# Performance work log

Measured on AMD Instinct MI355X. Metric: run time of the kernel, lower is better.

## Reference

```python
import jax, jax.numpy as jnp
import numpy as np

B, T, F, H = 2048, 256, 128, 64


def setup_inputs() -> dict:
    key = jax.random.key(0)
    ks = jax.random.split(key, 7)
    s_ih = 1.0 / np.sqrt(H)
    return {
        "x": jax.random.normal(ks[0], (B, T, F), dtype=jnp.float32),
        "w_ih": jax.random.uniform(ks[1], (3 * H, F), jnp.float32, -s_ih, s_ih),
        "w_hh": jax.random.uniform(ks[2], (3 * H, H), jnp.float32, -s_ih, s_ih),
        "b_ih": jax.random.uniform(ks[3], (3 * H,), jnp.float32, -s_ih, s_ih),
        "b_hh": jax.random.uniform(ks[4], (3 * H,), jnp.float32, -s_ih, s_ih),
        "fc_w": jax.random.uniform(ks[5], (1, H), jnp.float32, -s_ih, s_ih),
        "fc_b": jax.random.uniform(ks[6], (1,), jnp.float32, -s_ih, s_ih),
    }


def _gru_last_hidden(x, w_ih, w_hh, b_ih, b_hh):
    # Precompute input projections for all timesteps: [B,T,3H] -> scan over T
    gx = jnp.einsum("btf,gf->btg", x, w_ih) + b_ih  # g = 3H
    gx = jnp.transpose(gx, (1, 0, 2))  # [T, B, 3H]
    h0 = jnp.zeros((x.shape[0], w_hh.shape[1]), dtype=x.dtype)
    Hd = w_hh.shape[1]

    def step(h, gx_t):
        gh = h @ w_hh.T + b_hh  # [B, 3H]
        rx, zx, nx = gx_t[:, :Hd], gx_t[:, Hd:2 * Hd], gx_t[:, 2 * Hd:]
        rh, zh, nh = gh[:, :Hd], gh[:, Hd:2 * Hd], gh[:, 2 * Hd:]
        r = jax.nn.sigmoid(rx + rh)
        z = jax.nn.sigmoid(zx + zh)
        n = jnp.tanh(nx + r * nh)
        h_new = (1.0 - z) * n + z * h
        return h_new, None

    h_last, _ = jax.lax.scan(step, h0, gx)
    return h_last  # [B, H]


def reference(x, w_ih, w_hh, b_ih, b_hh, fc_w, fc_b):
    # eval mode: dropout is identity
    h_last = _gru_last_hidden(x, w_ih, w_hh, b_ih, b_hh)
    return h_last @ fc_w.T + fc_b  # [B, 1]
```

## Files before the change

kernel.cpp:

```cpp
#include <hip/hip_runtime.h>

#define B_ 2048
#define T_ 256
#define F_ 128
#define H_ 64

typedef __attribute__((ext_vector_type(8))) short short8;
typedef __attribute__((ext_vector_type(4))) float f32x4;

__device__ __forceinline__ unsigned int rne2(float fa, float fb) {
    unsigned int ua = __float_as_uint(fa);
    unsigned int ub = __float_as_uint(fb);
    ua = ua + 0x7fffu + ((ua >> 16) & 1u);
    ub = ub + 0x7fffu + ((ub >> 16) & 1u);
    return (ua >> 16) | (ub & 0xffff0000u);
}
__device__ __forceinline__ float sigmoid_f(float v) {
    return __fdividef(1.0f, 1.0f + __expf(-v));
}
__device__ __forceinline__ float tanh_f(float v) {
    return 1.0f - __fdividef(2.0f, 1.0f + __expf(2.0f * v));
}

__global__ __launch_bounds__(128, 2) void gru_fused(
    const float* __restrict__ x, const float* __restrict__ w_ih,
    const float* __restrict__ w_hh, const float* __restrict__ b_ih,
    const float* __restrict__ b_hh, const float* __restrict__ fc_w,
    const float* __restrict__ fc_b, float* __restrict__ out)
{
    __shared__ __align__(16) short wihf[12 * 4 * 64 * 8];
    __shared__ __align__(16) short whhf[12 * 2 * 64 * 8];
    __shared__ __align__(16) short hhi_l[2][4][72];
    __shared__ __align__(16) short hlo_l[2][4][72];
    __shared__ float wred[2][4];

    const int tid = threadIdx.x;
    const int wv  = tid >> 6;
    const int j   = tid & 63;
    const int q   = j >> 4;
    const int c   = j & 15;
    const int brow = blockIdx.x * 4;

    for (int s = tid; s < 12 * 4 * 64; s += 128) {
        const int n = s >> 8, ks = (s >> 6) & 3, L = s & 63;
        const float* wp = w_ih + (n * 16 + (L & 15)) * F_ + ks * 32 + ((L >> 4) * 8);
        const float4 a = *(const float4*)wp;
        const float4 b = *(const float4*)(wp + 4);
        union { short8 v; unsigned int u[4]; } fr;
        fr.u[0] = rne2(a.x, a.y); fr.u[1] = rne2(a.z, a.w);
        fr.u[2] = rne2(b.x, b.y); fr.u[3] = rne2(b.z, b.w);
        *(short8*)&wihf[s * 8] = fr.v;
    }
    for (int s = tid; s < 12 * 2 * 64; s += 128) {
        const int n = s >> 7, ks2 = (s >> 6) & 1, L = s & 63;
        const float* wp = w_hh + (n * 16 + (L & 15)) * H_ + ks2 * 32 + ((L >> 4) * 8);
        const float4 a = *(const float4*)wp;
        const float4 b = *(const float4*)(wp + 4);
        union { short8 v; unsigned int u[4]; } fr;
        fr.u[0] = rne2(a.x, a.y); fr.u[1] = rne2(a.z, a.w);
        fr.u[2] = rne2(b.x, b.y); fr.u[3] = rne2(b.z, b.w);
        *(short8*)&whhf[s * 8] = fr.v;
    }
    for (int i = tid; i < 2 * 4 * 72; i += 128) {
        ((short*)hhi_l)[i] = 0;
        ((short*)hlo_l)[i] = 0;
    }

    const int d0 = wv * 32 + c;
    float bxr[2], bxz[2], bxn[2], bgr[2], bgz[2], bgn[2];
    #pragma unroll
    for (int n2 = 0; n2 < 2; ++n2) {
        const int d = d0 + n2 * 16;
        bxr[n2] = b_ih[d];        bgr[n2] = b_hh[d];
        bxz[n2] = b_ih[64 + d];   bgz[n2] = b_hh[64 + d];
        bxn[n2] = b_ih[128 + d];  bgn[n2] = b_hh[128 + d];
    }
    const float fw0 = fc_w[d0], fw1 = fc_w[d0 + 16];

    const int xrow = (j & 15) & 3;
    const int xsl  = (j & 15) >> 3;
    const float* xlane = x + ((size_t)(brow + xrow) * T_ + xsl) * F_ + q * 8;

    __syncthreads();

    float4 XA[8], XB[8];
    {
        const float* lp = xlane;
        #pragma unroll
        for (int ks = 0; ks < 4; ++ks) {
            XA[2 * ks]     = *(const float4*)(lp + ks * 32);
            XA[2 * ks + 1] = *(const float4*)(lp + ks * 32 + 4);
        }
        lp = xlane + 2 * F_;
        #pragma unroll
        for (int ks = 0; ks < 4; ++ks) {
            XB[2 * ks]     = *(const float4*)(lp + ks * 32);
            XB[2 * ks + 1] = *(const float4*)(lp + ks * 32 + 4);
        }
    }

    short8 af[4], hh[2], hl[2];
    const short8 z8 = {0, 0, 0, 0, 0, 0, 0, 0};
    hh[0] = z8; hh[1] = z8; hl[0] = z8; hl[1] = z8;

    auto cvtbuf = [&](float4 (&Xv)[8]) {
        #pragma unroll
        for (int ks = 0; ks < 4; ++ks) {
            union { short8 v; unsigned int u[4]; } fr;
            fr.u[0] = rne2(Xv[2 * ks].x,     Xv[2 * ks].y);
            fr.u[1] = rne2(Xv[2 * ks].z,     Xv[2 * ks].w);
            fr.u[2] = rne2(Xv[2 * ks + 1].x, Xv[2 * ks + 1].y);
            fr.u[3] = rne2(Xv[2 * ks + 1].z, Xv[2 * ks + 1].w);
            af[ks] = fr.v;
        }
    };
    cvtbuf(XA);

    auto do_macro = [&](float4 (&Xre)[8], float4 (&Xcv)[8], int t0) {
        f32x4 axr[2], axz[2], axn[2];
        #pragma unroll
        for (int n2 = 0; n2 < 2; ++n2) {
            axr[n2] = (f32x4){bxr[n2], bxr[n2], bxr[n2], bxr[n2]};
            axz[n2] = (f32x4){bxz[n2], bxz[n2], bxz[n2], bxz[n2]};
            axn[n2] = (f32x4){bxn[n2], bxn[n2], bxn[n2], bxn[n2]};
            const int tr = (0 + wv * 2 + n2) * 2048;
            const int tz = (4 + wv * 2 + n2) * 2048;
            const int tn = (8 + wv * 2 + n2) * 2048;
            #pragma unroll
            for (int ks = 0; ks < 4; ++ks) {
                axr[n2] = __builtin_amdgcn_mfma_f32_16x16x32_bf16(
                    af[ks], *(const short8*)&wihf[tr + ks * 512 + j * 8], axr[n2], 0, 0, 0);
                axz[n2] = __builtin_amdgcn_mfma_f32_16x16x32_bf16(
                    af[ks], *(const short8*)&wihf[tz + ks * 512 + j * 8], axz[n2], 0, 0, 0);
                axn[n2] = __builtin_amdgcn_mfma_f32_16x16x32_bf16(
                    af[ks], *(const short8*)&wihf[tn + ks * 512 + j * 8], axn[n2], 0, 0, 0);
            }
        }
        {
            int tl = t0 + 4; if (tl > 254) tl = 254;
            const float* lp = xlane + (size_t)tl * F_;
            #pragma unroll
            for (int ks = 0; ks < 4; ++ks) {
                Xre[2 * ks]     = *(const float4*)(lp + ks * 32);
                Xre[2 * ks + 1] = *(const float4*)(lp + ks * 32 + 4);
            }
        }
        auto step = [&](int s) {
            f32x4 agr[2], agz[2], agn[2];
            #pragma unroll
            for (int n2 = 0; n2 < 2; ++n2) {
                agr[n2] = (f32x4){bgr[n2], bgr[n2], bgr[n2], bgr[n2]};
                agz[n2] = (f32x4){bgz[n2], bgz[n2], bgz[n2], bgz[n2]};
                agn[n2] = (f32x4){bgn[n2], bgn[n2], bgn[n2], bgn[n2]};
                const int tr = (0 + wv * 2 + n2) * 1024;
                const int tz = (4 + wv * 2 + n2) * 1024;
                const int tn = (8 + wv * 2 + n2) * 1024;
                #pragma unroll
                for (int ks2 = 0; ks2 < 2; ++ks2) {
                    const short8 br = *(const short8*)&whhf[tr + ks2 * 512 + j * 8];
                    const short8 bz = *(const short8*)&whhf[tz + ks2 * 512 + j * 8];
                    const short8 bn = *(const short8*)&whhf[tn + ks2 * 512 + j * 8];
                    agr[n2] = __builtin_amdgcn_mfma_f32_16x16x32_bf16(hh[ks2], br, agr[n2], 0, 0, 0);
                    agr[n2] = __builtin_amdgcn_mfma_f32_16x16x32_bf16(hl[ks2], br, agr[n2], 0, 0, 0);
                    agz[n2] = __builtin_amdgcn_mfma_f32_16x16x32_bf16(hh[ks2], bz, agz[n2], 0, 0, 0);
                    agz[n2] = __builtin_amdgcn_mfma_f32_16x16x32_bf16(hl[ks2], bz, agz[n2], 0, 0, 0);
                    agn[n2] = __builtin_amdgcn_mfma_f32_16x16x32_bf16(hh[ks2], bn, agn[n2], 0, 0, 0);
                    agn[n2] = __builtin_amdgcn_mfma_f32_16x16x32_bf16(hl[ks2], bn, agn[n2], 0, 0, 0);
                }
            }
            if ((q >> 1) == s) {
                const int rowsel = q & 1;
                #pragma unroll
                for (int n2 = 0; n2 < 2; ++n2) {
                    const int d = d0 + n2 * 16;
                    #pragma unroll
                    for (int rl = 0; rl < 2; ++rl) {
                        const int row = rowsel * 2 + rl;
                        const float vr  = rowsel ? axr[n2][2 + rl] + agr[n2][2 + rl]
                                                 : axr[n2][rl]     + agr[n2][rl];
                        const float vz  = rowsel ? axz[n2][2 + rl] + agz[n2][2 + rl]
                                                 : axz[n2][rl]     + agz[n2][rl];
                        const float vnx = rowsel ? axn[n2][2 + rl] : axn[n2][rl];
                        const float vnh = rowsel ? agn[n2][2 + rl] : agn[n2][rl];
                        const float r = sigmoid_f(vr);
                        const float z = sigmoid_f(vz);
                        const float n = tanh_f(vnx + r * vnh);
                        const float hp =
                            __uint_as_float(((unsigned int)(unsigned short)hhi_l[s][row][d]) << 16) +
                            __uint_as_float(((unsigned int)(unsigned short)hlo_l[s][row][d]) << 16);
                        const float hn = n + z * (hp - n);
                        const unsigned int uh = __float_as_uint(hn);
                        const unsigned int rr = uh + 0x7fffu + ((uh >> 16) & 1u);
                        const float hif = __uint_as_float(rr & 0xffff0000u);
                        const float lof = hn - hif;
                        const unsigned int ul = __float_as_uint(lof);
                        const unsigned int r2 = ul + 0x7fffu + ((ul >> 16) & 1u);
                        hhi_l[s ^ 1][row][d] = (short)(rr >> 16);
                        hlo_l[s ^ 1][row][d] = (short)(r2 >> 16);
                    }
                }
            }
            __syncthreads();
            #pragma unroll
            for (int ks2 = 0; ks2 < 2; ++ks2) {
                hh[ks2] = *(const short8*)&hhi_l[s ^ 1][xrow][ks2 * 32 + q * 8];
                hl[ks2] = *(const short8*)&hlo_l[s ^ 1][xrow][ks2 * 32 + q * 8];
            }
        };
        step(0);
        step(1);
        cvtbuf(Xcv);
    };

    #pragma unroll 1
    for (int t0 = 0; t0 < T_; t0 += 4) {
        do_macro(XA, XB, t0);
        do_macro(XB, XA, t0 + 2);
    }

    {
        const int row = q;
        const float hv0 =
            __uint_as_float(((unsigned int)(unsigned short)hhi_l[0][row][d0]) << 16) +
            __uint_as_float(((unsigned int)(unsigned short)hlo_l[0][row][d0]) << 16);
        const float hv1 =
            __uint_as_float(((unsigned int)(unsigned short)hhi_l[0][row][d0 + 16]) << 16) +
            __uint_as_float(((unsigned int)(unsigned short)hlo_l[0][row][d0 + 16]) << 16);
        float partial = hv0 * fw0 + hv1 * fw1;
        #pragma unroll
        for (int m = 1; m <= 8; m <<= 1) partial += __shfl_xor(partial, m, 64);
        if (c == 0) wred[wv][q] = partial;
        __syncthreads();
        if (tid < 4) out[brow + tid] = wred[0][tid] + wred[1][tid] + fc_b[0];
    }
}

extern "C" void kernel_launch(void* const* d_in, const int* in_sizes, int n_in,
                              void* d_out, int out_size, void* d_ws, size_t ws_size,
                              hipStream_t stream)
{
    (void)in_sizes; (void)n_in; (void)out_size; (void)d_ws; (void)ws_size;
    const float* x    = (const float*)d_in[0];
    const float* w_ih = (const float*)d_in[1];
    const float* w_hh = (const float*)d_in[2];
    const float* b_ih = (const float*)d_in[3];
    const float* b_hh = (const float*)d_in[4];
    const float* fc_w = (const float*)d_in[5];
    const float* fc_b = (const float*)d_in[6];
    float* out = (float*)d_out;

    gru_fused<<<dim3(B_ / 4), 128, 0, stream>>>(
        x, w_ih, w_hh, b_ih, b_hh, fc_w, fc_b, out);
}
```

Measured before the change: 631.0 us.

## Split hidden dim across four waves and keep W_hh fragments in registers

```diff
diff --git a/kernel.cpp b/kernel.cpp
--- a/kernel.cpp
+++ b/kernel.cpp
@@ -22,17 +22,16 @@
     return 1.0f - __fdividef(2.0f, 1.0f + __expf(2.0f * v));
 }
 
-__global__ __launch_bounds__(128, 2) void gru_fused(
+__global__ __launch_bounds__(256, 2) void gru_fused(
     const float* __restrict__ x, const float* __restrict__ w_ih,
     const float* __restrict__ w_hh, const float* __restrict__ b_ih,
     const float* __restrict__ b_hh, const float* __restrict__ fc_w,
     const float* __restrict__ fc_b, float* __restrict__ out)
 {
     __shared__ __align__(16) short wihf[12 * 4 * 64 * 8];
-    __shared__ __align__(16) short whhf[12 * 2 * 64 * 8];
     __shared__ __align__(16) short hhi_l[2][4][72];
     __shared__ __align__(16) short hlo_l[2][4][72];
-    __shared__ float wred[2][4];
+    __shared__ float wred[4][4];
 
     const int tid = threadIdx.x;
     const int wv  = tid >> 6;
@@ -41,7 +40,7 @@
     const int c   = j & 15;
     const int brow = blockIdx.x * 4;
 
-    for (int s = tid; s < 12 * 4 * 64; s += 128) {
+    for (int s = tid; s < 12 * 4 * 64; s += 256) {
         const int n = s >> 8, ks = (s >> 6) & 3, L = s & 63;
         const float* wp = w_ih + (n * 16 + (L & 15)) * F_ + ks * 32 + ((L >> 4) * 8);
         const float4 a = *(const float4*)wp;
@@ -51,31 +50,31 @@
         fr.u[2] = rne2(b.x, b.y); fr.u[3] = rne2(b.z, b.w);
         *(short8*)&wihf[s * 8] = fr.v;
     }
-    for (int s = tid; s < 12 * 2 * 64; s += 128) {
-        const int n = s >> 7, ks2 = (s >> 6) & 1, L = s & 63;
-        const float* wp = w_hh + (n * 16 + (L & 15)) * H_ + ks2 * 32 + ((L >> 4) * 8);
-        const float4 a = *(const float4*)wp;
-        const float4 b = *(const float4*)(wp + 4);
-        union { short8 v; unsigned int u[4]; } fr;
-        fr.u[0] = rne2(a.x, a.y); fr.u[1] = rne2(a.z, a.w);
-        fr.u[2] = rne2(b.x, b.y); fr.u[3] = rne2(b.z, b.w);
-        *(short8*)&whhf[s * 8] = fr.v;
-    }
-    for (int i = tid; i < 2 * 4 * 72; i += 128) {
+    for (int i = tid; i < 2 * 4 * 72; i += 256) {
         ((short*)hhi_l)[i] = 0;
         ((short*)hlo_l)[i] = 0;
     }
 
-    const int d0 = wv * 32 + c;
-    float bxr[2], bxz[2], bxn[2], bgr[2], bgz[2], bgn[2];
+    const int d0 = wv * 16 + c;
+    const float bxr = b_ih[d0],       bgr = b_hh[d0];
+    const float bxz = b_ih[64 + d0],  bgz = b_hh[64 + d0];
+    const float bxn = b_ih[128 + d0], bgn = b_hh[128 + d0];
+    const float fw0 = fc_w[d0];
+
+    short8 wh[3][2];
     #pragma unroll
-    for (int n2 = 0; n2 < 2; ++n2) {
-        const int d = d0 + n2 * 16;
-        bxr[n2] = b_ih[d];        bgr[n2] = b_hh[d];
-        bxz[n2] = b_ih[64 + d];   bgz[n2] = b_hh[64 + d];
-        bxn[n2] = b_ih[128 + d];  bgn[n2] = b_hh[128 + d];
-    }
-    const float fw0 = fc_w[d0], fw1 = fc_w[d0 + 16];
+    for (int g = 0; g < 3; ++g) {
+        #pragma unroll
+        for (int ks2 = 0; ks2 < 2; ++ks2) {
+            const float* wp = w_hh + (g * 64 + wv * 16 + c) * H_ + ks2 * 32 + q * 8;
+            const float4 a = *(const float4*)wp;
+            const float4 b = *(const float4*)(wp + 4);
+            union { short8 v; unsigned int u[4]; } fr;
+            fr.u[0] = rne2(a.x, a.y); fr.u[1] = rne2(a.z, a.w);
+            fr.u[2] = rne2(b.x, b.y); fr.u[3] = rne2(b.z, b.w);
+            wh[g][ks2] = fr.v;
+        }
+    }
 
     const int xrow = (j & 15) & 3;
     const int xsl  = (j & 15) >> 3;
@@ -117,23 +116,21 @@
     cvtbuf(XA);
 
     auto do_macro = [&](float4 (&Xre)[8], float4 (&Xcv)[8], int t0) {
-        f32x4 axr[2], axz[2], axn[2];
-        #pragma unroll
-        for (int n2 = 0; n2 < 2; ++n2) {
-            axr[n2] = (f32x4){bxr[n2], bxr[n2], bxr[n2], bxr[n2]};
-            axz[n2] = (f32x4){bxz[n2], bxz[n2], bxz[n2], bxz[n2]};
-            axn[n2] = (f32x4){bxn[n2], bxn[n2], bxn[n2], bxn[n2]};
-            const int tr = (0 + wv * 2 + n2) * 2048;
-            const int tz = (4 + wv * 2 + n2) * 2048;
-            const int tn = (8 + wv * 2 + n2) * 2048;
+        f32x4 axr = {bxr, bxr, bxr, bxr};
+        f32x4 axz = {bxz, bxz, bxz, bxz};
+        f32x4 axn = {bxn, bxn, bxn, bxn};
+        {
+            const int tr = (0 + wv) * 2048;
+            const int tz = (4 + wv) * 2048;
+            const int tn = (8 + wv) * 2048;
             #pragma unroll
             for (int ks = 0; ks < 4; ++ks) {
-                axr[n2] = __builtin_amdgcn_mfma_f32_16x16x32_bf16(
-                    af[ks], *(const short8*)&wihf[tr + ks * 512 + j * 8], axr[n2], 0, 0, 0);
-                axz[n2] = __builtin_amdgcn_mfma_f32_16x16x32_bf16(
-                    af[ks], *(const short8*)&wihf[tz + ks * 512 + j * 8], axz[n2], 0, 0, 0);
-                axn[n2] = __builtin_amdgcn_mfma_f32_16x16x32_bf16(
-                    af[ks], *(const short8*)&wihf[tn + ks * 512 + j * 8], axn[n2], 0, 0, 0);
+                axr = __builtin_amdgcn_mfma_f32_16x16x32_bf16(
+                    af[ks], *(const short8*)&wihf[tr + ks * 512 + j * 8], axr, 0, 0, 0);
+                axz = __builtin_amdgcn_mfma_f32_16x16x32_bf16(
+                    af[ks], *(const short8*)&wihf[tz + ks * 512 + j * 8], axz, 0, 0, 0);
+                axn = __builtin_amdgcn_mfma_f32_16x16x32_bf16(
+                    af[ks], *(const short8*)&wihf[tn + ks * 512 + j * 8], axn, 0, 0, 0);
             }
         }
         {
@@ -146,58 +143,41 @@
             }
         }
         auto step = [&](int s) {
-            f32x4 agr[2], agz[2], agn[2];
-            #pragma unroll
-            for (int n2 = 0; n2 < 2; ++n2) {
-                agr[n2] = (f32x4){bgr[n2], bgr[n2], bgr[n2], bgr[n2]};
-                agz[n2] = (f32x4){bgz[n2], bgz[n2], bgz[n2], bgz[n2]};
-                agn[n2] = (f32x4){bgn[n2], bgn[n2], bgn[n2], bgn[n2]};
-                const int tr = (0 + wv * 2 + n2) * 1024;
-                const int tz = (4 + wv * 2 + n2) * 1024;
-                const int tn = (8 + wv * 2 + n2) * 1024;
-                #pragma unroll
-                for (int ks2 = 0; ks2 < 2; ++ks2) {
-                    const short8 br = *(const short8*)&whhf[tr + ks2 * 512 + j * 8];
-                    const short8 bz = *(const short8*)&whhf[tz + ks2 * 512 + j * 8];
-                    const short8 bn = *(const short8*)&whhf[tn + ks2 * 512 + j * 8];
-                    agr[n2] = __builtin_amdgcn_mfma_f32_16x16x32_bf16(hh[ks2], br, agr[n2], 0, 0, 0);
-                    agr[n2] = __builtin_amdgcn_mfma_f32_16x16x32_bf16(hl[ks2], br, agr[n2], 0, 0, 0);
-                    agz[n2] = __builtin_amdgcn_mfma_f32_16x16x32_bf16(hh[ks2], bz, agz[n2], 0, 0, 0);
-                    agz[n2] = __builtin_amdgcn_mfma_f32_16x16x32_bf16(hl[ks2], bz, agz[n2], 0, 0, 0);
-                    agn[n2] = __builtin_amdgcn_mfma_f32_16x16x32_bf16(hh[ks2], bn, agn[n2], 0, 0, 0);
-                    agn[n2] = __builtin_amdgcn_mfma_f32_16x16x32_bf16(hl[ks2], bn, agn[n2], 0, 0, 0);
-                }
+            f32x4 agr = {bgr, bgr, bgr, bgr};
+            f32x4 agz = {bgz, bgz, bgz, bgz};
+            f32x4 agn = {bgn, bgn, bgn, bgn};
+            #pragma unroll
+            for (int ks2 = 0; ks2 < 2; ++ks2) {
+                agr = __builtin_amdgcn_mfma_f32_16x16x32_bf16(hh[ks2], wh[0][ks2], agr, 0, 0, 0);
+                agr = __builtin_amdgcn_mfma_f32_16x16x32_bf16(hl[ks2], wh[0][ks2], agr, 0, 0, 0);
+                agz = __builtin_amdgcn_mfma_f32_16x16x32_bf16(hh[ks2], wh[1][ks2], agz, 0, 0, 0);
+                agz = __builtin_amdgcn_mfma_f32_16x16x32_bf16(hl[ks2], wh[1][ks2], agz, 0, 0, 0);
+                agn = __builtin_amdgcn_mfma_f32_16x16x32_bf16(hh[ks2], wh[2][ks2], agn, 0, 0, 0);
+                agn = __builtin_amdgcn_mfma_f32_16x16x32_bf16(hl[ks2], wh[2][ks2], agn, 0, 0, 0);
             }
             if ((q >> 1) == s) {
                 const int rowsel = q & 1;
                 #pragma unroll
-                for (int n2 = 0; n2 < 2; ++n2) {
-                    const int d = d0 + n2 * 16;
-                    #pragma unroll
-                    for (int rl = 0; rl < 2; ++rl) {
-                        const int row = rowsel * 2 + rl;
-                        const float vr  = rowsel ? axr[n2][2 + rl] + agr[n2][2 + rl]
-                                                 : axr[n2][rl]     + agr[n2][rl];
-                        const float vz  = rowsel ? axz[n2][2 + rl] + agz[n2][2 + rl]
-                                                 : axz[n2][rl]     + agz[n2][rl];
-                        const float vnx = rowsel ? axn[n2][2 + rl] : axn[n2][rl];
-                        const float vnh = rowsel ? agn[n2][2 + rl] : agn[n2][rl];
-                        const float r = sigmoid_f(vr);
-                        const float z = sigmoid_f(vz);
-                        const float n = tanh_f(vnx + r * vnh);
-                        const float hp =
-                            __uint_as_float(((unsigned int)(unsigned short)hhi_l[s][row][d]) << 16) +
-                            __uint_as_float(((unsigned int)(unsigned short)hlo_l[s][row][d]) << 16);
-                        const float hn = n + z * (hp - n);
-                        const unsigned int uh = __float_as_uint(hn);
-                        const unsigned int rr = uh + 0x7fffu + ((uh >> 16) & 1u);
-                        const float hif = __uint_as_float(rr & 0xffff0000u);
-                        const float lof = hn - hif;
-                        const unsigned int ul = __float_as_uint(lof);
-                        const unsigned int r2 = ul + 0x7fffu + ((ul >> 16) & 1u);
-                        hhi_l[s ^ 1][row][d] = (short)(rr >> 16);
-                        hlo_l[s ^ 1][row][d] = (short)(r2 >> 16);
-                    }
+                for (int rl = 0; rl < 2; ++rl) {
+                    const int row = rowsel * 2 + rl;
+                    const int e   = rowsel * 2 + rl;
+                    const float vr  = axr[e] + agr[e];
+                    const float vz  = axz[e] + agz[e];
+                    const float r = sigmoid_f(vr);
+                    const float z = sigmoid_f(vz);
+                    const float n = tanh_f(axn[e] + r * agn[e]);
+                    const float hp =
+                        __uint_as_float(((unsigned int)(unsigned short)hhi_l[s][row][d0]) << 16) +
+                        __uint_as_float(((unsigned int)(unsigned short)hlo_l[s][row][d0]) << 16);
+                    const float hn = n + z * (hp - n);
+                    const unsigned int uh = __float_as_uint(hn);
+                    const unsigned int rr = uh + 0x7fffu + ((uh >> 16) & 1u);
+                    const float hif = __uint_as_float(rr & 0xffff0000u);
+                    const float lof = hn - hif;
+                    const unsigned int ul = __float_as_uint(lof);
+                    const unsigned int r2 = ul + 0x7fffu + ((ul >> 16) & 1u);
+                    hhi_l[s ^ 1][row][d0] = (short)(rr >> 16);
+                    hlo_l[s ^ 1][row][d0] = (short)(r2 >> 16);
                 }
             }
             __syncthreads();
@@ -223,15 +203,13 @@
         const float hv0 =
             __uint_as_float(((unsigned int)(unsigned short)hhi_l[0][row][d0]) << 16) +
             __uint_as_float(((unsigned int)(unsigned short)hlo_l[0][row][d0]) << 16);
-        const float hv1 =
-            __uint_as_float(((unsigned int)(unsigned short)hhi_l[0][row][d0 + 16]) << 16) +
-            __uint_as_float(((unsigned int)(unsigned short)hlo_l[0][row][d0 + 16]) << 16);
-        float partial = hv0 * fw0 + hv1 * fw1;
+        float partial = hv0 * fw0;
         #pragma unroll
         for (int m = 1; m <= 8; m <<= 1) partial += __shfl_xor(partial, m, 64);
         if (c == 0) wred[wv][q] = partial;
         __syncthreads();
-        if (tid < 4) out[brow + tid] = wred[0][tid] + wred[1][tid] + fc_b[0];
+        if (tid < 4)
+            out[brow + tid] = wred[0][tid] + wred[1][tid] + wred[2][tid] + wred[3][tid] + fc_b[0];
     }
 }
 
@@ -249,6 +227,6 @@
     const float* fc_b = (const float*)d_in[6];
     float* out = (float*)d_out;
 
-    gru_fused<<<dim3(B_ / 4), 128, 0, stream>>>(
+    gru_fused<<<dim3(B_ / 4), 256, 0, stream>>>(
         x, w_ih, w_hh, b_ih, b_hh, fc_w, fc_b, out);
 }
```

New measurement: 582.2 us. 1.08x faster.
